# Kernel optimization log

Hardware: AMD Instinct MI355X
Metric: run time of the kernel (lower is better)

## Reference

```python
import jax, jax.numpy as jnp
import numpy as np

NH = 32          # nh * 2 neighbors per point (init nh=16)
P_REDUCTION = 0.5


def setup_inputs() -> dict:
    key = jax.random.key(0)
    k1, k2 = jax.random.split(key)
    x = jax.random.normal(k1, (2, 8192, 256), dtype=jnp.float32)       # [b, n, e]
    coords = jax.random.normal(k2, (2, 2, 8192, 1), dtype=jnp.float32) # [b, c, n, 1]
    return {"x": x, "coords": coords}


def _knn_gather(x, coords):
    """Return features of the NH nearest neighbors of each point: [b, n, NH, e]."""
    cs = coords[..., 0]                                   # [b, c, n]
    sq = jnp.sum(cs * cs, axis=1)                         # [b, n]
    # squared euclidean distances [b, n, n]
    d2 = sq[:, :, None] + sq[:, None, :] - 2.0 * jnp.einsum('bcn,bcm->bnm', cs, cs)
    d2 = jax.lax.stop_gradient(d2)                        # indices are non-differentiable
    _, nn_idx = jax.lax.top_k(-d2, NH)                    # [b, n, NH] nearest points
    # gather neighbor features: [b, 1, n, e] indexed with [b, n, NH, 1] -> [b, n, NH, e]
    x_nh = jnp.take_along_axis(x[:, None, :, :], nn_idx[..., None], axis=2)
    return x_nh


def _forward(x, coords):
    b, n, e = x.shape
    x_nh = _knn_gather(x, coords)                         # [b, n, NH, e]
    # unbiased std over the neighbor dim (torch.std default, ddof=1)
    mean_nh = jnp.mean(x_nh, axis=-2, keepdims=True)
    local_s = jnp.sqrt(jnp.sum((x_nh - mean_nh) ** 2, axis=-2) / (NH - 1))  # [b, n, e]
    global_m = jnp.abs(jnp.mean(x, axis=1))               # [b, e]
    local_dist = jnp.sum(local_s / global_m[:, None, :], axis=-1)           # [b, n]
    n_keep = int((1.0 - P_REDUCTION) * n)
    _, keep_idx = jax.lax.top_k(local_dist, n_keep)       # [b, n_keep], sorted desc
    x_out = jnp.take_along_axis(x, keep_idx[:, :, None], axis=1)            # [b, n_keep, e]
    coords_out = jnp.take_along_axis(coords, keep_idx[:, None, :, None], axis=2)  # [b, c, n_keep, 1]
    return x_out, coords_out, local_dist


def reference(x, coords):
    return _forward(x, coords)
```

## Files before the change

kernel.cpp:

```cpp
#include <hip/hip_runtime.h>

#define NN 8192
#define EE 256
#define KNH 32
#define NKEEP 4096
#define NCX 64
#define NCELL 4096
#define CNT_MIN 48

typedef unsigned long long u64;
typedef unsigned int u32;


__device__ __forceinline__ int cellof(float v) {
    const int q = (int)floorf((v + 4.6f) * (64.0f / 9.2f));
    return min(max(q, 0), NCX - 1);
}

__global__ void k_gm_partial(const float* __restrict__ x, float* __restrict__ part) {
    const int b = blockIdx.y, chunk = blockIdx.x, t = threadIdx.x;
    const float* xp = x + ((size_t)b * NN + (size_t)chunk * 256) * EE + t;
    float s = 0.0f;
    for (int i = 0; i < 256; ++i) s += xp[(size_t)i * EE];
    part[((size_t)b * 32 + chunk) * EE + t] = s;
}

__global__ void k_gm_final(const float* __restrict__ part, float* __restrict__ gm) {
    const int b = blockIdx.y, t = threadIdx.x;
    float s = 0.0f;
    for (int c = 0; c < 32; ++c) s += part[((size_t)b * 32 + c) * EE + t];
    gm[b * EE + t] = fabsf(s / (float)NN);
}

__global__ void __launch_bounds__(1024) k_binning(const float* __restrict__ coords,
                                                  int* __restrict__ start,
                                                  float2* __restrict__ sc,
                                                  int* __restrict__ sj) {
    __shared__ int cnt[NCELL];
    __shared__ int ps[1024];
    const int b = blockIdx.x, t = threadIdx.x;
#pragma unroll
    for (int k = 0; k < 4; ++k) cnt[k * 1024 + t] = 0;
    __syncthreads();
#pragma unroll
    for (int k = 0; k < 8; ++k) {
        const int i = k * 1024 + t;
        const float xv = coords[(size_t)b * 2 * NN + i];
        const float yv = coords[(size_t)b * 2 * NN + NN + i];
        atomicAdd(&cnt[cellof(xv) * NCX + cellof(yv)], 1);
    }
    __syncthreads();
    const int v0 = cnt[t * 4 + 0], v1 = cnt[t * 4 + 1];
    const int v2 = cnt[t * 4 + 2], v3 = cnt[t * 4 + 3];
    const int s = v0 + v1 + v2 + v3;
    ps[t] = s;
    __syncthreads();
    for (int d = 1; d < 1024; d <<= 1) {
        const int add = (t >= d) ? ps[t - d] : 0;
        __syncthreads();
        ps[t] += add;
        __syncthreads();
    }
    int run = ps[t] - s;
    start[b * (NCELL + 1) + t * 4 + 0] = run; cnt[t * 4 + 0] = run; run += v0;
    start[b * (NCELL + 1) + t * 4 + 1] = run; cnt[t * 4 + 1] = run; run += v1;
    start[b * (NCELL + 1) + t * 4 + 2] = run; cnt[t * 4 + 2] = run; run += v2;
    start[b * (NCELL + 1) + t * 4 + 3] = run; cnt[t * 4 + 3] = run; run += v3;
    if (t == 0) start[b * (NCELL + 1) + NCELL] = NN;
    __syncthreads();
#pragma unroll
    for (int k = 0; k < 8; ++k) {
        const int i = k * 1024 + t;
        const float xv = coords[(size_t)b * 2 * NN + i];
        const float yv = coords[(size_t)b * 2 * NN + NN + i];
        const int p = atomicAdd(&cnt[cellof(xv) * NCX + cellof(yv)], 1);
        sc[(size_t)b * NN + p] = make_float2(xv, yv);
        sj[(size_t)b * NN + p] = i;
    }
}

__device__ __forceinline__ u64 shfl_xor_u64(u64 v, int m) {
    const u32 hi = (u32)__shfl_xor((int)(u32)(v >> 32), m);
    const u32 lo = (u32)__shfl_xor((int)(u32)v, m);
    return ((u64)hi << 32) | lo;
}

__device__ __forceinline__ u64 wave_min_u64(u64 h) {
#pragma unroll
    for (int s = 1; s < 64; s <<= 1) {
        const u64 o = shfl_xor_u64(h, s);
        h = (o < h) ? o : h;
    }
    return h;
}

__global__ void __launch_bounds__(256) k_knn_dist(
        const float* __restrict__ x,
        const float* __restrict__ gm, const float2* __restrict__ sc,
        const int* __restrict__ sj, const int* __restrict__ start,
        float* __restrict__ ld_out) {
    __shared__ u64 comp[4][64];
    const int wg   = blockIdx.x;
    const int swz  = (wg & 7) * 512 + (wg >> 3);
    const int b    = swz >> 11;
    const int pb   = swz & 2047;
    const int wid  = threadIdx.x >> 6;
    const int lane = threadIdx.x & 63;
    const int p    = pb * 4 + wid;

    const float2* scb = sc + (size_t)b * NN;
    const int*    sjb = sj + (size_t)b * NN;
    const int*    stb = start + b * (NCELL + 1);
    const float2 cp = scb[p];
    const int    i  = sjb[p];
    const float ci0 = cp.x, ci1 = cp.y;
    const int qx = cellof(ci0), qy = cellof(ci1);

    int r = 1, xl, yl, yh, nsl;
    int myc0 = 0, mylen = 0;
    for (;;) {
        xl = max(qx - r, 0);
        const int xh = min(qx + r, NCX - 1);
        yl = max(qy - r, 0);
        yh = min(qy + r, NCX - 1);
        nsl = xh - xl + 1;
        int c0 = 0, c1 = 0;
        if (lane < nsl) {
            c0 = stb[(xl + lane) * NCX + yl];
            c1 = stb[(xl + lane) * NCX + yh + 1];
        }
        myc0 = c0; mylen = c1 - c0;
        int tot = mylen;
#pragma unroll
        for (int s = 1; s < 64; s <<= 1) tot += __shfl_xor(tot, s);
        if (tot >= CNT_MIN || r >= NCX) break;
        r <<= 1;
    }
    int incl = mylen;
#pragma unroll
    for (int d = 1; d < 64; d <<= 1) {
        const int v = __shfl_up(incl, d);
        incl += (lane >= d) ? v : 0;
    }
    int excl = incl - mylen;
    const int L1 = __shfl(incl, 63);

    float dmin = 1e30f;
    for (int g = 0; g < L1; g += 64) {
        const int gp = g + lane;
        int lo = 0, hi = nsl - 1;
#pragma unroll
        for (int st = 0; st < 6; ++st) {
            const int mid = (lo + hi + 1) >> 1;
            const int v = __shfl(excl, mid);
            const bool go = (v <= gp);
            lo = go ? mid : lo;
            hi = go ? hi : mid - 1;
        }
        const int cnd = __shfl(myc0, lo) + gp - __shfl(excl, lo);
        const int cc  = min(max(cnd, 0), NN - 1);
        const float2 pt = scb[cc];
        const float dx = ci0 - pt.x, dy = ci1 - pt.y;
        const float d  = fmaf(dx, dx, dy * dy);
        if (gp < L1) dmin = fminf(dmin, d);
    }

    u32 mk = __float_as_uint(dmin);
#pragma unroll
    for (int k = 2; k <= 64; k <<= 1) {
#pragma unroll
        for (int j = k >> 1; j > 0; j >>= 1) {
            const u32 o = (u32)__shfl_xor((int)mk, j);
            const bool keep_min = (((lane & j) == 0) == ((lane & k) == 0));
            const u32 mn = min(mk, o), mx = max(mk, o);
            mk = keep_min ? mn : mx;
        }
    }
    const u32 T = (u32)__shfl((int)mk, 31);

    const float srad = sqrtf(__uint_as_float(T)) * 1.0002f + 1e-5f;
    xl = cellof(ci0 - srad);
    const int xh2 = cellof(ci0 + srad);
    yl = cellof(ci1 - srad);
    yh = cellof(ci1 + srad);
    nsl = xh2 - xl + 1;
    {
        int c0 = 0, c1 = 0;
        if (lane < nsl) {
            c0 = stb[(xl + lane) * NCX + yl];
            c1 = stb[(xl + lane) * NCX + yh + 1];
        }
        myc0 = c0; mylen = c1 - c0;
    }
    incl = mylen;
#pragma unroll
    for (int d = 1; d < 64; d <<= 1) {
        const int v = __shfl_up(incl, d);
        incl += (lane >= d) ? v : 0;
    }
    excl = incl - mylen;
    const int L2 = __shfl(incl, 63);

    const u64 lmask = (1ull << lane) - 1;
    int base = 0;
    for (int g = 0; g < L2; g += 64) {
        const int gp = g + lane;
        int lo = 0, hi = nsl - 1;
#pragma unroll
        for (int st = 0; st < 6; ++st) {
            const int mid = (lo + hi + 1) >> 1;
            const int v = __shfl(excl, mid);
            const bool go = (v <= gp);
            lo = go ? mid : lo;
            hi = go ? hi : mid - 1;
        }
        const int cnd = __shfl(myc0, lo) + gp - __shfl(excl, lo);
        const int cc  = min(max(cnd, 0), NN - 1);
        const float2 pt = scb[cc];
        const int    jj = sjb[cc];
        const float dx = ci0 - pt.x, dy = ci1 - pt.y;
        const u32 db = __float_as_uint(fmaf(dx, dx, dy * dy));
        const bool keep = (gp < L2) && (db <= T);
        const u64 m = __ballot(keep);
        const int pos = base + __popcll(m & lmask);
        base += __popcll(m);
        if (keep && pos < 64) comp[wid][pos] = ((u64)db << 32) | (u32)jj;
    }
    const bool ovf = (base > 64) || (base < KNH);

    u64 key = (lane < base) ? comp[wid][lane] : ~0ull;
#pragma unroll
    for (int k = 2; k <= 64; k <<= 1) {
#pragma unroll
        for (int j = k >> 1; j > 0; j >>= 1) {
            const u64 other = shfl_xor_u64(key, j);
            const bool keep_min = (((lane & j) == 0) == ((lane & k) == 0));
            const bool lt = (key < other);
            const u64 mn = lt ? key : other;
            const u64 mx = lt ? other : key;
            key = keep_min ? mn : mx;
        }
    }
    int jkeep = (int)(u32)key;

    if (ovf) {
        u64 minkeep = 0;
        for (int k = 0; k < KNH; ++k) {
            u64 best = ~0ull;
            for (int g = 0; g < L2; g += 64) {
                const int gp = g + lane;
                int lo = 0, hi = nsl - 1;
#pragma unroll
                for (int st = 0; st < 6; ++st) {
                    const int mid = (lo + hi + 1) >> 1;
                    const int v = __shfl(excl, mid);
                    const bool go = (v <= gp);
                    lo = go ? mid : lo;
                    hi = go ? hi : mid - 1;
                }
                const int cnd = __shfl(myc0, lo) + gp - __shfl(excl, lo);
                const int cc  = min(max(cnd, 0), NN - 1);
                const float2 pt = scb[cc];
                const int    jj = sjb[cc];
                const float dx = ci0 - pt.x, dy = ci1 - pt.y;
                const float d  = fmaf(dx, dx, dy * dy);
                const u64 kk = ((u64)__float_as_uint(d) << 32) | (u32)jj;
                if (gp < L2 && kk >= minkeep && kk < best) best = kk;
            }
            const u64 h = wave_min_u64(best);
            if (lane == k) jkeep = (int)(u32)h;
            minkeep = h + 1;
        }
    }

    float s1[4] = {0.f, 0.f, 0.f, 0.f};
    float s2[4] = {0.f, 0.f, 0.f, 0.f};
    const float* xb = x + (size_t)b * NN * EE;
#pragma unroll 8
    for (int k = 0; k < KNH; ++k) {
        const int j = __builtin_amdgcn_readlane(jkeep, k);
        const float4 v = *reinterpret_cast<const float4*>(xb + (size_t)j * EE + (lane << 2));
        s1[0] += v.x; s2[0] += v.x * v.x;
        s1[1] += v.y; s2[1] += v.y * v.y;
        s1[2] += v.z; s2[2] += v.z * v.z;
        s1[3] += v.w; s2[3] += v.w * v.w;
    }

    const float* gmb = gm + b * EE;
    float tt = 0.f;
#pragma unroll
    for (int q = 0; q < 4; ++q) {
        const float sum = s1[q];
        float ssd = s2[q] - sum * sum * (1.0f / 32.0f);
        ssd = ssd > 0.f ? ssd : 0.f;
        const float ls = sqrtf(ssd * (1.0f / 31.0f));
        tt += ls / gmb[(lane << 2) + q];
    }
#pragma unroll
    for (int s2r = 1; s2r < 64; s2r <<= 1) tt += __shfl_xor(tt, s2r);

    if (lane == 0) ld_out[(size_t)b * NN + i] = tt;
}

__global__ void k_rank_gather(const float* __restrict__ x, const float* __restrict__ coords,
                              const float* __restrict__ ld,
                              float* __restrict__ x_out, float* __restrict__ c_out) {
    const int b    = blockIdx.y;
    const int wid  = threadIdx.x >> 6;
    const int lane = threadIdx.x & 63;
    const int i    = blockIdx.x * 4 + wid;
    const float* lb = ld + (size_t)b * NN;
    const float di = lb[i];
    int cnt = 0;
    for (int t = 0; t < NN / 64; ++t) {
        const int j = lane + t * 64;
        const float dj = lb[j];
        cnt += (dj > di || (dj == di && j < i)) ? 1 : 0;
    }
#pragma unroll
    for (int s = 1; s < 64; s <<= 1) cnt += __shfl_xor(cnt, s);

    if (cnt < NKEEP) {
        const float4 v = *reinterpret_cast<const float4*>(x + ((size_t)b * NN + i) * EE + (lane << 2));
        *reinterpret_cast<float4*>(x_out + ((size_t)b * NKEEP + cnt) * EE + (lane << 2)) = v;
        if (lane < 2) {
            c_out[((size_t)b * 2 + lane) * NKEEP + cnt] = coords[((size_t)b * 2 + lane) * NN + i];
        }
    }
}

extern "C" void kernel_launch(void* const* d_in, const int* in_sizes, int n_in,
                              void* d_out, int out_size, void* d_ws, size_t ws_size,
                              hipStream_t stream) {
    const float* x      = (const float*)d_in[0];
    const float* coords = (const float*)d_in[1];

    float* out    = (float*)d_out;
    float* x_out  = out;
    float* c_out  = out + 2097152;
    float* ld_out = out + 2113536;

    char*   ws    = (char*)d_ws;
    float*  part  = (float*)(ws);
    float*  gm    = (float*)(ws + 65536);
    int*    start = (int*)  (ws + 67584);
    float2* sc    = (float2*)(ws + 100384);
    int*    sj    = (int*)  (ws + 231456);

    k_binning    <<<2,             1024, 0, stream>>>(coords, start, sc, sj);
    k_gm_partial <<<dim3(32, 2),   256,  0, stream>>>(x, part);
    k_gm_final   <<<dim3(1, 2),    256,  0, stream>>>(part, gm);
    k_knn_dist   <<<4096,          256,  0, stream>>>(x, gm, sc, sj, start, ld_out);
    k_rank_gather<<<dim3(2048, 2), 256,  0, stream>>>(x, coords, ld_out, x_out, c_out);
}
```

Baseline: 99.04 us.

## Fuse binning with global-mean partials, use wave scan, vectorize rank counting

Merges the binning kernel and the global-mean partial-sum kernel into one launch, with extra blocks computing the column partials so both run concurrently. The block-wide Hillis-Steele scan with many barriers is replaced by a wave-level shuffle scan plus a per-wave sum combine. The rank-counting loop in the gather kernel now loads four distances per lane as float4, cutting load instruction count. These trim launch overhead and small serial kernels; the fused kernel mixes divergent roles within one grid.

Result: faster. 86.25 us (-12.9%).

```diff
diff --git a/kernel.cpp b/kernel.cpp
--- a/kernel.cpp
+++ b/kernel.cpp
@@ -17,28 +17,28 @@
     return min(max(q, 0), NCX - 1);
 }
 
-__global__ void k_gm_partial(const float* __restrict__ x, float* __restrict__ part) {
-    const int b = blockIdx.y, chunk = blockIdx.x, t = threadIdx.x;
-    const float* xp = x + ((size_t)b * NN + (size_t)chunk * 256) * EE + t;
-    float s = 0.0f;
-    for (int i = 0; i < 256; ++i) s += xp[(size_t)i * EE];
-    part[((size_t)b * 32 + chunk) * EE + t] = s;
-}
-
-__global__ void k_gm_final(const float* __restrict__ part, float* __restrict__ gm) {
-    const int b = blockIdx.y, t = threadIdx.x;
-    float s = 0.0f;
-    for (int c = 0; c < 32; ++c) s += part[((size_t)b * 32 + c) * EE + t];
-    gm[b * EE + t] = fabsf(s / (float)NN);
-}
-
-__global__ void __launch_bounds__(1024) k_binning(const float* __restrict__ coords,
-                                                  int* __restrict__ start,
-                                                  float2* __restrict__ sc,
-                                                  int* __restrict__ sj) {
+__global__ void __launch_bounds__(1024) k_pre(const float* __restrict__ coords,
+                                              const float* __restrict__ x,
+                                              int* __restrict__ start,
+                                              float2* __restrict__ sc,
+                                              int* __restrict__ sj,
+                                              float* __restrict__ part) {
     __shared__ int cnt[NCELL];
-    __shared__ int ps[1024];
-    const int b = blockIdx.x, t = threadIdx.x;
+    __shared__ int wsum[16];
+    const int blk = blockIdx.x;
+    if (blk >= 2) {
+        const int unit  = (blk - 2) * 4 + (threadIdx.x >> 8);
+        const int b     = unit >> 5;
+        const int chunk = unit & 31;
+        const int t     = threadIdx.x & 255;
+        const float* xp = x + ((size_t)b * NN + (size_t)chunk * 256) * EE + t;
+        float s = 0.0f;
+        for (int i = 0; i < 256; ++i) s += xp[(size_t)i * EE];
+        part[((size_t)b * 32 + chunk) * EE + t] = s;
+        return;
+    }
+    const int b = blk, t = threadIdx.x;
+    const int lane = t & 63, wv = t >> 6;
 #pragma unroll
     for (int k = 0; k < 4; ++k) cnt[k * 1024 + t] = 0;
     __syncthreads();
@@ -53,15 +53,18 @@
     const int v0 = cnt[t * 4 + 0], v1 = cnt[t * 4 + 1];
     const int v2 = cnt[t * 4 + 2], v3 = cnt[t * 4 + 3];
     const int s = v0 + v1 + v2 + v3;
-    ps[t] = s;
+    int inc = s;
+#pragma unroll
+    for (int d = 1; d < 64; d <<= 1) {
+        const int u = __shfl_up(inc, d);
+        inc += (lane >= d) ? u : 0;
+    }
+    if (lane == 63) wsum[wv] = inc;
     __syncthreads();
-    for (int d = 1; d < 1024; d <<= 1) {
-        const int add = (t >= d) ? ps[t - d] : 0;
-        __syncthreads();
-        ps[t] += add;
-        __syncthreads();
-    }
-    int run = ps[t] - s;
+    int wpre = 0;
+#pragma unroll
+    for (int w = 0; w < 16; ++w) wpre += (w < wv) ? wsum[w] : 0;
+    int run = wpre + inc - s;
     start[b * (NCELL + 1) + t * 4 + 0] = run; cnt[t * 4 + 0] = run; run += v0;
     start[b * (NCELL + 1) + t * 4 + 1] = run; cnt[t * 4 + 1] = run; run += v1;
     start[b * (NCELL + 1) + t * 4 + 2] = run; cnt[t * 4 + 2] = run; run += v2;
@@ -77,6 +80,13 @@
         sc[(size_t)b * NN + p] = make_float2(xv, yv);
         sj[(size_t)b * NN + p] = i;
     }
+}
+
+__global__ void k_gm_final(const float* __restrict__ part, float* __restrict__ gm) {
+    const int b = blockIdx.y, t = threadIdx.x;
+    float s = 0.0f;
+    for (int c = 0; c < 32; ++c) s += part[((size_t)b * 32 + c) * EE + t];
+    gm[b * EE + t] = fabsf(s / (float)NN);
 }
 
 __device__ __forceinline__ u64 shfl_xor_u64(u64 v, int m) {
@@ -312,10 +322,13 @@
     const float* lb = ld + (size_t)b * NN;
     const float di = lb[i];
     int cnt = 0;
-    for (int t = 0; t < NN / 64; ++t) {
-        const int j = lane + t * 64;
-        const float dj = lb[j];
-        cnt += (dj > di || (dj == di && j < i)) ? 1 : 0;
+    for (int t = 0; t < NN / 256; ++t) {
+        const int j0 = t * 256 + (lane << 2);
+        const float4 dv = *reinterpret_cast<const float4*>(lb + j0);
+        cnt += (dv.x > di || (dv.x == di && (j0 + 0) < i)) ? 1 : 0;
+        cnt += (dv.y > di || (dv.y == di && (j0 + 1) < i)) ? 1 : 0;
+        cnt += (dv.z > di || (dv.z == di && (j0 + 2) < i)) ? 1 : 0;
+        cnt += (dv.w > di || (dv.w == di && (j0 + 3) < i)) ? 1 : 0;
     }
 #pragma unroll
     for (int s = 1; s < 64; s <<= 1) cnt += __shfl_xor(cnt, s);
@@ -347,8 +360,7 @@
     float2* sc    = (float2*)(ws + 100384);
     int*    sj    = (int*)  (ws + 231456);
 
-    k_binning    <<<2,             1024, 0, stream>>>(coords, start, sc, sj);
-    k_gm_partial <<<dim3(32, 2),   256,  0, stream>>>(x, part);
+    k_pre        <<<18,            1024, 0, stream>>>(coords, x, start, sc, sj, part);
     k_gm_final   <<<dim3(1, 2),    256,  0, stream>>>(part, gm);
     k_knn_dist   <<<4096,          256,  0, stream>>>(x, gm, sc, sj, start, ld_out);
     k_rank_gather<<<dim3(2048, 2), 256,  0, stream>>>(x, coords, ld_out, x_out, c_out);
```
